# Kernel optimization log

Measured on AMD Instinct MI355X. Metric: run time of the kernel, lower is better.

Reference implementation:

```python
import jax, jax.numpy as jnp
import numpy as np

N_NODES = 100000
N_EDGES = 1600000
R_DIM = 8      # radial_embedding_dim (j)
L_DIM = 4      # angular dim (l)
C_DIM = 8      # channel_dim (k)
CUTOFF = 5.5
MP_NORM_FACTOR = 1.0


def setup_inputs() -> dict:
    key = jax.random.key(0)
    k1, k2, k3, k4, k5, k6, k7 = jax.random.split(key, 7)
    node_feat = jax.random.normal(k1, (N_NODES, R_DIM, L_DIM, C_DIM), dtype=jnp.float32)
    edge_lengths = jax.random.uniform(k2, (N_EDGES,), dtype=jnp.float32) * CUTOFF
    radial_cutoff_fn = jax.random.uniform(k3, (N_EDGES,), dtype=jnp.float32)
    edge_index = jax.random.randint(k4, (2, N_EDGES), 0, N_NODES, dtype=jnp.int64)
    prefactor = jax.random.uniform(k5, (R_DIM, C_DIM), dtype=jnp.float32)
    invr0 = (jax.random.uniform(k6, (R_DIM, C_DIM), dtype=jnp.float32) + 0.5) / CUTOFF
    memory_coef = jnp.float32(0.25)
    return {
        "node_feat": node_feat,
        "edge_lengths": edge_lengths,
        "radial_cutoff_fn": radial_cutoff_fn,
        "edge_index": edge_index,
        "prefactor": prefactor,
        "invr0": invr0,
        "memory_coef": memory_coef,
    }


def reference(node_feat, edge_lengths, radial_cutoff_fn, edge_index, prefactor, invr0, memory_coef):
    n_nodes = node_feat.shape[0]
    # radial decay: [E, R, C] = exp(-len * invr0) * prefactor * cutoff_fn
    radial_decay = (
        jnp.exp(-edge_lengths[:, None, None] * invr0)
        * prefactor
        * radial_cutoff_fn[:, None, None]
    )
    # gather sender features [E, R, L, C] and modulate per (edge, radial, channel)
    sender = node_feat[edge_index[0]]
    message = sender * radial_decay[:, :, None, :]
    # scatter-sum messages to receiver nodes
    agg = jax.ops.segment_sum(message, edge_index[1], num_segments=n_nodes)
    return node_feat * memory_coef + agg * MP_NORM_FACTOR
```

## Files before the change

kernel.cpp:

```cpp
#include <hip/hip_runtime.h>
#include <hip/hip_fp16.h>

#define RLC 256
#define BUCKET 32
#define OVF_CAP 65536
#define SCAN_BLOCK 256
#define SCAN_ITEMS 4

__device__ __forceinline__ float fast_exp2(float x) {
#if __has_builtin(__builtin_amdgcn_exp2f)
    return __builtin_amdgcn_exp2f(x);
#else
    return __expf(x * 0.6931471805599453f);
#endif
}

__device__ __forceinline__ unsigned int bfr(float f) {
    unsigned int u = __float_as_uint(f);
    return (u + 0x7fffu + ((u >> 16) & 1u)) >> 16;
}

#define LOG2E 1.4426950408889634f


__global__ __launch_bounds__(256) void cast_t_kernel(
    const float4* __restrict__ in, uint2* __restrict__ outp, int nr)
{
    int i = blockIdx.x * blockDim.x + threadIdx.x;
    if (i >= nr) return;
    const float4* p = in + (size_t)i * 8;
    float v[32];
    #pragma unroll
    for (int q = 0; q < 8; ++q) {
        float4 t = p[q];
        v[4*q+0] = t.x; v[4*q+1] = t.y; v[4*q+2] = t.z; v[4*q+3] = t.w;
    }
    uint2* o = outp + (size_t)i * 8;
    #pragma unroll
    for (int c = 0; c < 8; ++c) {
        unsigned int lo = bfr(v[0*8+c]) | (bfr(v[1*8+c]) << 16);
        unsigned int hi = bfr(v[2*8+c]) | (bfr(v[3*8+c]) << 16);
        o[c] = make_uint2(lo, hi);
    }
}

__global__ __launch_bounds__(256) void build_kernel(
    const int* __restrict__ edge_index,
    const float* __restrict__ edge_len,
    const float* __restrict__ cutoff_fn,
    int* __restrict__ counts,
    int2* __restrict__ payload,
    int4* __restrict__ ovf,
    int* __restrict__ ovf_cnt,
    int n_edges)
{
    int e = blockIdx.x * blockDim.x + threadIdx.x;
    if (e >= n_edges) return;
    int dst = edge_index[n_edges + e];
    int src = edge_index[e];
    unsigned int hnl = __half_as_ushort(__float2half(-edge_len[e]));
    unsigned int hcf = __half_as_ushort(__float2half(cutoff_fn[e]));
    int pk = (int)((hcf << 16) | hnl);
    int r = atomicAdd(&counts[dst], 1);
    if (r < BUCKET) {
        payload[(size_t)dst * BUCKET + r] = make_int2(src, pk);
    } else {
        int o = atomicAdd(ovf_cnt, 1);
        if (o < OVF_CAP) ovf[o] = make_int4(dst, src, pk, 0);
    }
}

__global__ __launch_bounds__(256) void gather_bucket_kernel(
    const float* __restrict__ node_feat,
    const unsigned short* __restrict__ nfbT,
    const int2* __restrict__ payload,
    const float* __restrict__ prefactor,
    const float* __restrict__ invr0,
    const float* __restrict__ coef_p,
    const int* __restrict__ counts,
    float* __restrict__ out,
    int n_nodes)
{
    __shared__ float4 slot[4][BUCKET];
    int wave = threadIdx.x >> 6;
    int lane = threadIdx.x & 63;
    int node = blockIdx.x * 4 + wave;
    bool valid = node < n_nodes;

    float iv = invr0[lane] * LOG2E;
    float pf = prefactor[lane];
    float coef = *coef_p;

    int r = lane >> 3, c = lane & 7;
    long obase = (long)node * RLC + r * 32 + c;

    float a0 = 0.f, a1 = 0.f, a2 = 0.f, a3 = 0.f;
    int m = 0;
    if (valid) {
        int deg = counts[node];
        m = deg < BUCKET ? deg : BUCKET;
        a0 = node_feat[obase]      * coef;
        a1 = node_feat[obase + 8]  * coef;
        a2 = node_feat[obase + 16] * coef;
        a3 = node_feat[obase + 24] * coef;
        if (lane < m) {
            int2 p = payload[(size_t)node * BUCKET + lane];
            float nl = __half2float(__ushort_as_half((unsigned short)(p.y & 0xffff)));
            float cf = __half2float(__ushort_as_half((unsigned short)(((unsigned int)p.y) >> 16)));
            slot[wave][lane] = make_float4(__int_as_float(p.x), nl, cf, 0.f);
        }
    }
    __syncthreads();

    if (valid) {
        #pragma unroll 4
        for (int it = 0; it < m; ++it) {
            float4 s = slot[wave][it];
            int src = __float_as_int(s.x);
            float w = fast_exp2(s.y * iv) * pf * s.z;
            uint2 raw = *(const uint2*)(nfbT + (size_t)src * RLC + lane * 4);
            float f0 = __uint_as_float(raw.x << 16);
            float f1 = __uint_as_float(raw.x & 0xffff0000u);
            float f2 = __uint_as_float(raw.y << 16);
            float f3 = __uint_as_float(raw.y & 0xffff0000u);
            a0 += w * f0; a1 += w * f1; a2 += w * f2; a3 += w * f3;
        }
        out[obase]      = a0;
        out[obase + 8]  = a1;
        out[obase + 16] = a2;
        out[obase + 24] = a3;
    }
}

__global__ __launch_bounds__(256) void ovf_kernel(
    const unsigned short* __restrict__ nfbT,
    const float* __restrict__ prefactor,
    const float* __restrict__ invr0,
    const int4* __restrict__ ovf,
    const int* __restrict__ ovf_cnt,
    float* __restrict__ out)
{
    int gtid = blockIdx.x * blockDim.x + threadIdx.x;
    int wid  = gtid >> 6;
    int lane = gtid & 63;
    int nwaves = (gridDim.x * blockDim.x) >> 6;
    int n = *ovf_cnt;
    if (n > OVF_CAP) n = OVF_CAP;

    float iv = invr0[lane] * LOG2E;
    float pf = prefactor[lane];
    int r = lane >> 3, c = lane & 7;

    for (int i = wid; i < n; i += nwaves) {
        int4 rec = ovf[i];
        int dst = rec.x, src = rec.y, pk = rec.z;
        float nl = __half2float(__ushort_as_half((unsigned short)(pk & 0xffff)));
        float cf = __half2float(__ushort_as_half((unsigned short)(((unsigned int)pk) >> 16)));
        float w = fast_exp2(nl * iv) * pf * cf;
        uint2 raw = *(const uint2*)(nfbT + (size_t)src * RLC + lane * 4);
        float f0 = __uint_as_float(raw.x << 16);
        float f1 = __uint_as_float(raw.x & 0xffff0000u);
        float f2 = __uint_as_float(raw.y << 16);
        float f3 = __uint_as_float(raw.y & 0xffff0000u);
        float* o = out + (long)dst * RLC + r * 32 + c;
        atomicAdd(o,      w * f0);
        atomicAdd(o + 8,  w * f1);
        atomicAdd(o + 16, w * f2);
        atomicAdd(o + 24, w * f3);
    }
}


__global__ __launch_bounds__(256) void cast_kernel(
    const float4* __restrict__ in, uint4* __restrict__ outp, int n8)
{
    int i = blockIdx.x * blockDim.x + threadIdx.x;
    if (i >= n8) return;
    float4 a = in[2 * i];
    float4 b = in[2 * i + 1];
    uint4 r;
    r.x = bfr(a.x) | (bfr(a.y) << 16);
    r.y = bfr(a.z) | (bfr(a.w) << 16);
    r.z = bfr(b.x) | (bfr(b.y) << 16);
    r.w = bfr(b.z) | (bfr(b.w) << 16);
    outp[i] = r;
}

__global__ __launch_bounds__(256) void hist_rank_kernel(
    const int* __restrict__ edge_index, int* __restrict__ counts,
    unsigned char* __restrict__ rank, int n_edges)
{
    int e = blockIdx.x * blockDim.x + threadIdx.x;
    if (e >= n_edges) return;
    int dst = edge_index[n_edges + e];
    int r = atomicAdd(&counts[dst], 1);
    rank[e] = (unsigned char)r;
}

__global__ __launch_bounds__(SCAN_BLOCK) void scan1_kernel(
    const int* __restrict__ in, int* __restrict__ out,
    int* __restrict__ blocksums, int n)
{
    __shared__ int tmp[SCAN_BLOCK];
    int t = threadIdx.x;
    int base = blockIdx.x * SCAN_BLOCK * SCAN_ITEMS + t * SCAN_ITEMS;
    int v[SCAN_ITEMS];
    int tot = 0;
    #pragma unroll
    for (int k = 0; k < SCAN_ITEMS; ++k) {
        int i = base + k;
        v[k] = (i < n) ? in[i] : 0;
        tot += v[k];
    }
    tmp[t] = tot;
    __syncthreads();
    int run = tot;
    for (int d = 1; d < SCAN_BLOCK; d <<= 1) {
        int x = (t >= d) ? tmp[t - d] : 0;
        __syncthreads();
        tmp[t] += x;
        __syncthreads();
    }
    int excl = tmp[t] - run;
    #pragma unroll
    for (int k = 0; k < SCAN_ITEMS; ++k) {
        int i = base + k;
        if (i < n) out[i] = excl;
        excl += v[k];
    }
    if (t == SCAN_BLOCK - 1) blocksums[blockIdx.x] = tmp[t];
}

__global__ __launch_bounds__(SCAN_BLOCK) void scan2_kernel(
    int* __restrict__ blocksums, int nb)
{
    __shared__ int tmp[SCAN_BLOCK];
    int t = threadIdx.x;
    int v = (t < nb) ? blocksums[t] : 0;
    tmp[t] = v;
    __syncthreads();
    for (int d = 1; d < SCAN_BLOCK; d <<= 1) {
        int x = (t >= d) ? tmp[t - d] : 0;
        __syncthreads();
        tmp[t] += x;
        __syncthreads();
    }
    if (t < nb) blocksums[t] = tmp[t] - v;
}

__global__ __launch_bounds__(256) void scan3_kernel(
    int* __restrict__ offsets, const int* __restrict__ blocksums,
    int n, int n_edges)
{
    int i = blockIdx.x * blockDim.x + threadIdx.x;
    if (i == 0) offsets[n] = n_edges;
    if (i >= n) return;
    offsets[i] += blocksums[i / (SCAN_BLOCK * SCAN_ITEMS)];
}

__global__ __launch_bounds__(256) void scatter_rank_kernel(
    const int* __restrict__ edge_index,
    const float* __restrict__ edge_len,
    const float* __restrict__ cutoff_fn,
    const int* __restrict__ offsets,
    const unsigned char* __restrict__ rank,
    int2* __restrict__ payload, int n_edges)
{
    int e = blockIdx.x * blockDim.x + threadIdx.x;
    if (e >= n_edges) return;
    int dst = edge_index[n_edges + e];
    int src = edge_index[e];
    unsigned int hnl = __half_as_ushort(__float2half(-edge_len[e]));
    unsigned int hcf = __half_as_ushort(__float2half(cutoff_fn[e]));
    int pos = offsets[dst] + (int)rank[e];
    payload[pos] = make_int2(src, (int)((hcf << 16) | hnl));
}

__global__ __launch_bounds__(256) void gather_kernel(
    const float* __restrict__ node_feat,
    const unsigned short* __restrict__ nfb,
    const int2* __restrict__ payload,
    const float* __restrict__ prefactor,
    const float* __restrict__ invr0,
    const float* __restrict__ coef_p,
    const int*  __restrict__ offsets,
    float* __restrict__ out,
    int n_nodes)
{
    int tid  = blockIdx.x * blockDim.x + threadIdx.x;
    int node = tid >> 6;
    int lane = threadIdx.x & 63;
    if (node >= n_nodes) return;

    int f0     = lane << 2;
    int rcbase = ((f0 >> 5) << 3) + (f0 & 7);

    float4 iv = *(const float4*)(invr0 + rcbase);
    iv.x *= LOG2E; iv.y *= LOG2E; iv.z *= LOG2E; iv.w *= LOG2E;
    const float4 pf = *(const float4*)(prefactor + rcbase);
    float coef = *coef_p;

    const float4 self = *(const float4*)(node_feat + (long)node * RLC + f0);
    float ax = self.x * coef, ay = self.y * coef,
          az = self.z * coef, aw = self.w * coef;

    int j   = offsets[node];
    int end = offsets[node + 1];

    for (int base = j; base < end; base += 64) {
        int idx = base + lane;
        int2 p = make_int2(0, 0);
        if (idx < end) p = payload[idx];
        int m = end - base;
        if (m > 64) m = 64;
        int psrc = p.x;
        int ppk  = p.y;

        #pragma unroll 4
        for (int it = 0; it < m; ++it) {
            int src = __shfl(psrc, it, 64);
            int pk  = __shfl(ppk,  it, 64);
            float nl = __half2float(__ushort_as_half((unsigned short)(pk & 0xffff)));
            float cf = __half2float(__ushort_as_half((unsigned short)(((unsigned int)pk) >> 16)));
            uint2 raw = *(const uint2*)(nfb + (long)src * RLC + f0);
            float fx = __uint_as_float(raw.x << 16);
            float fy = __uint_as_float(raw.x & 0xffff0000u);
            float fz = __uint_as_float(raw.y << 16);
            float fw = __uint_as_float(raw.y & 0xffff0000u);
            ax += fx * (fast_exp2(nl * iv.x) * pf.x * cf);
            ay += fy * (fast_exp2(nl * iv.y) * pf.y * cf);
            az += fz * (fast_exp2(nl * iv.z) * pf.z * cf);
            aw += fw * (fast_exp2(nl * iv.w) * pf.w * cf);
        }
    }

    *(float4*)(out + (long)node * RLC + f0) = make_float4(ax, ay, az, aw);
}

__global__ __launch_bounds__(256) void init_out_kernel(
    const float4* __restrict__ nf4, float4* __restrict__ out4,
    const float* __restrict__ coef_p, int n4)
{
    int i = blockIdx.x * blockDim.x + threadIdx.x;
    if (i >= n4) return;
    float c = *coef_p;
    float4 v = nf4[i];
    out4[i] = make_float4(v.x * c, v.y * c, v.z * c, v.w * c);
}

__global__ __launch_bounds__(256) void edge_scatter_kernel(
    const float* __restrict__ node_feat,
    const float* __restrict__ edge_len,
    const float* __restrict__ cutoff_fn,
    const int*  __restrict__ edge_index,
    const float* __restrict__ prefactor,
    const float* __restrict__ invr0,
    float* __restrict__ out, int n_edges)
{
    int tid  = blockIdx.x * blockDim.x + threadIdx.x;
    int e    = tid >> 6;
    int lane = threadIdx.x & 63;
    if (e >= n_edges) return;
    int   src = edge_index[e];
    int   dst = edge_index[n_edges + e];
    float len = edge_len[e];
    float cf  = cutoff_fn[e];
    int f0     = lane << 2;
    int rcbase = ((f0 >> 5) << 3) + (f0 & 7);
    const float4 iv = *(const float4*)(invr0 + rcbase);
    const float4 pf = *(const float4*)(prefactor + rcbase);
    const float4 s  = *(const float4*)(node_feat + (long)src * RLC + f0);
    float nl = -len;
    float* o = out + (long)dst * RLC + f0;
    atomicAdd(o + 0, s.x * __expf(nl * iv.x) * pf.x * cf);
    atomicAdd(o + 1, s.y * __expf(nl * iv.y) * pf.y * cf);
    atomicAdd(o + 2, s.z * __expf(nl * iv.z) * pf.z * cf);
    atomicAdd(o + 3, s.w * __expf(nl * iv.w) * pf.w * cf);
}

extern "C" void kernel_launch(void* const* d_in, const int* in_sizes, int n_in,
                              void* d_out, int out_size, void* d_ws, size_t ws_size,
                              hipStream_t stream) {
    const float* node_feat  = (const float*)d_in[0];
    const float* edge_len   = (const float*)d_in[1];
    const float* cutoff_fn  = (const float*)d_in[2];
    const int*   edge_index = (const int*)d_in[3];
    const float* prefactor  = (const float*)d_in[4];
    const float* invr0      = (const float*)d_in[5];
    const float* coef_p     = (const float*)d_in[6];
    float* out = (float*)d_out;

    const int n_edges = in_sizes[1];
    const int n_feat  = in_sizes[0];
    const int n_nodes = n_feat / RLC;

    size_t need1 = (size_t)n_feat * 2
                 + (size_t)n_nodes * BUCKET * 8
                 + (size_t)OVF_CAP * 16
                 + (size_t)(n_nodes + 1) * 4;

    const int per_block = SCAN_BLOCK * SCAN_ITEMS;
    const int nb1 = (n_nodes + per_block - 1) / per_block;
    size_t need2 = (size_t)n_feat * 2
                 + (size_t)n_edges * 8
                 + ((size_t)(n_nodes + 1) + n_nodes + 256) * 4
                 + (size_t)n_edges;

    if (ws_size >= need1) {
        unsigned short* nfbT = (unsigned short*)d_ws;
        int2* payload = (int2*)(nfbT + n_feat);
        int4* ovf     = (int4*)(payload + (size_t)n_nodes * BUCKET);
        int*  counts  = (int*)(ovf + OVF_CAP);
        int*  ovf_cnt = counts + n_nodes;

        int nr = n_nodes * 8;
        cast_t_kernel<<<(nr + 255) / 256, 256, 0, stream>>>(
            (const float4*)node_feat, (uint2*)nfbT, nr);

        (void)hipMemsetAsync(counts, 0, (size_t)(n_nodes + 1) * sizeof(int), stream);

        int eg = (n_edges + 255) / 256;
        build_kernel<<<eg, 256, 0, stream>>>(
            edge_index, edge_len, cutoff_fn, counts, payload, ovf, ovf_cnt, n_edges);

        int gg = (n_nodes + 3) / 4;
        gather_bucket_kernel<<<gg, 256, 0, stream>>>(
            node_feat, nfbT, payload, prefactor, invr0, coef_p, counts,
            out, n_nodes);

        ovf_kernel<<<64, 256, 0, stream>>>(
            nfbT, prefactor, invr0, ovf, ovf_cnt, out);
    } else if (ws_size >= need2 && nb1 <= SCAN_BLOCK) {
        unsigned short* nfb = (unsigned short*)d_ws;
        int2* payload   = (int2*)(nfb + n_feat);
        int* offsets    = (int*)(payload + n_edges);
        int* counts     = offsets + (n_nodes + 1);
        int* blocksums  = counts + n_nodes;
        unsigned char* rank = (unsigned char*)(blocksums + 256);

        int n8 = n_feat / 8;
        cast_kernel<<<(n8 + 255) / 256, 256, 0, stream>>>(
            (const float4*)node_feat, (uint4*)nfb, n8);

        (void)hipMemsetAsync(counts, 0, (size_t)n_nodes * sizeof(int), stream);

        int eg = (n_edges + 255) / 256;
        hist_rank_kernel<<<eg, 256, 0, stream>>>(edge_index, counts, rank, n_edges);
        scan1_kernel<<<nb1, SCAN_BLOCK, 0, stream>>>(counts, offsets, blocksums, n_nodes);
        scan2_kernel<<<1, SCAN_BLOCK, 0, stream>>>(blocksums, nb1);
        int ng = (n_nodes + 255) / 256;
        scan3_kernel<<<ng, 256, 0, stream>>>(offsets, blocksums, n_nodes, n_edges);
        scatter_rank_kernel<<<eg, 256, 0, stream>>>(
            edge_index, edge_len, cutoff_fn, offsets, rank, payload, n_edges);

        long total = (long)n_nodes * 64;
        int gg = (int)((total + 255) / 256);
        gather_kernel<<<gg, 256, 0, stream>>>(
            node_feat, nfb, payload, prefactor, invr0, coef_p, offsets,
            out, n_nodes);
    } else {
        int n4 = n_feat / 4;
        init_out_kernel<<<(n4 + 255) / 256, 256, 0, stream>>>(
            (const float4*)node_feat, (float4*)out, coef_p, n4);
        long total_threads = (long)n_edges * 64;
        int grid = (int)((total_threads + 255) / 256);
        edge_scatter_kernel<<<grid, 256, 0, stream>>>(
            node_feat, edge_len, cutoff_fn, edge_index,
            prefactor, invr0, out, n_edges);
    }
}
```

Measured before the change: 443.0 us.

## Merge cast and bucket-build kernels; drop LDS staging and use nontemporal accesses

The bf16 transpose-cast kernel and the edge bucket-build kernel now run as one launch, with blocks split by index range, so the two independent passes overlap and one launch disappears. In the gather kernel the shared-memory slot staging and the block-wide barrier are removed. Each wave now reads its payload entries directly inside the loop, and waves past the node count exit early. Streaming loads and stores are marked nontemporal to keep them from polluting cache, at the cost of more redundant payload loads per lane and less cache retention for the edge arrays.

```diff
diff --git a/kernel.cpp b/kernel.cpp
--- a/kernel.cpp
+++ b/kernel.cpp
@@ -23,28 +23,7 @@
 #define LOG2E 1.4426950408889634f
 
 
-__global__ __launch_bounds__(256) void cast_t_kernel(
-    const float4* __restrict__ in, uint2* __restrict__ outp, int nr)
-{
-    int i = blockIdx.x * blockDim.x + threadIdx.x;
-    if (i >= nr) return;
-    const float4* p = in + (size_t)i * 8;
-    float v[32];
-    #pragma unroll
-    for (int q = 0; q < 8; ++q) {
-        float4 t = p[q];
-        v[4*q+0] = t.x; v[4*q+1] = t.y; v[4*q+2] = t.z; v[4*q+3] = t.w;
-    }
-    uint2* o = outp + (size_t)i * 8;
-    #pragma unroll
-    for (int c = 0; c < 8; ++c) {
-        unsigned int lo = bfr(v[0*8+c]) | (bfr(v[1*8+c]) << 16);
-        unsigned int hi = bfr(v[2*8+c]) | (bfr(v[3*8+c]) << 16);
-        o[c] = make_uint2(lo, hi);
-    }
-}
-
-__global__ __launch_bounds__(256) void build_kernel(
+__global__ __launch_bounds__(256) void build_cast_kernel(
     const int* __restrict__ edge_index,
     const float* __restrict__ edge_len,
     const float* __restrict__ cutoff_fn,
@@ -52,21 +31,49 @@
     int2* __restrict__ payload,
     int4* __restrict__ ovf,
     int* __restrict__ ovf_cnt,
-    int n_edges)
-{
-    int e = blockIdx.x * blockDim.x + threadIdx.x;
-    if (e >= n_edges) return;
-    int dst = edge_index[n_edges + e];
-    int src = edge_index[e];
-    unsigned int hnl = __half_as_ushort(__float2half(-edge_len[e]));
-    unsigned int hcf = __half_as_ushort(__float2half(cutoff_fn[e]));
-    int pk = (int)((hcf << 16) | hnl);
-    int r = atomicAdd(&counts[dst], 1);
-    if (r < BUCKET) {
-        payload[(size_t)dst * BUCKET + r] = make_int2(src, pk);
+    int n_edges,
+    const float4* __restrict__ nf_in,
+    uint2* __restrict__ nfbT,
+    int nr,
+    int nb_build)
+{
+    if ((int)blockIdx.x < nb_build) {
+        int e = blockIdx.x * 256 + threadIdx.x;
+        if (e >= n_edges) return;
+        int dst = __builtin_nontemporal_load(edge_index + n_edges + e);
+        int src = __builtin_nontemporal_load(edge_index + e);
+        float  el = __builtin_nontemporal_load(edge_len + e);
+        float  cf = __builtin_nontemporal_load(cutoff_fn + e);
+        unsigned int hnl = __half_as_ushort(__float2half(-el));
+        unsigned int hcf = __half_as_ushort(__float2half(cf));
+        unsigned int pk = (hcf << 16) | hnl;
+        int r = atomicAdd(&counts[dst], 1);
+        if (r < BUCKET) {
+            unsigned long long v =
+                ((unsigned long long)pk << 32) | (unsigned int)src;
+            __builtin_nontemporal_store(
+                v, (unsigned long long*)&payload[(size_t)dst * BUCKET + r]);
+        } else {
+            int o = atomicAdd(ovf_cnt, 1);
+            if (o < OVF_CAP) ovf[o] = make_int4(dst, src, (int)pk, 0);
+        }
     } else {
-        int o = atomicAdd(ovf_cnt, 1);
-        if (o < OVF_CAP) ovf[o] = make_int4(dst, src, pk, 0);
+        int i = (blockIdx.x - nb_build) * 256 + threadIdx.x;
+        if (i >= nr) return;
+        const float4* p = nf_in + (size_t)i * 8;
+        float v[32];
+        #pragma unroll
+        for (int q = 0; q < 8; ++q) {
+            float4 t = p[q];
+            v[4*q+0] = t.x; v[4*q+1] = t.y; v[4*q+2] = t.z; v[4*q+3] = t.w;
+        }
+        uint2* o = nfbT + (size_t)i * 8;
+        #pragma unroll
+        for (int c = 0; c < 8; ++c) {
+            unsigned int lo = bfr(v[0*8+c]) | (bfr(v[1*8+c]) << 16);
+            unsigned int hi = bfr(v[2*8+c]) | (bfr(v[3*8+c]) << 16);
+            o[c] = make_uint2(lo, hi);
+        }
     }
 }
 
@@ -81,11 +88,10 @@
     float* __restrict__ out,
     int n_nodes)
 {
-    __shared__ float4 slot[4][BUCKET];
     int wave = threadIdx.x >> 6;
     int lane = threadIdx.x & 63;
     int node = blockIdx.x * 4 + wave;
-    bool valid = node < n_nodes;
+    if (node >= n_nodes) return;
 
     float iv = invr0[lane] * LOG2E;
     float pf = prefactor[lane];
@@ -94,42 +100,37 @@
     int r = lane >> 3, c = lane & 7;
     long obase = (long)node * RLC + r * 32 + c;
 
-    float a0 = 0.f, a1 = 0.f, a2 = 0.f, a3 = 0.f;
-    int m = 0;
-    if (valid) {
-        int deg = counts[node];
-        m = deg < BUCKET ? deg : BUCKET;
-        a0 = node_feat[obase]      * coef;
-        a1 = node_feat[obase + 8]  * coef;
-        a2 = node_feat[obase + 16] * coef;
-        a3 = node_feat[obase + 24] * coef;
-        if (lane < m) {
-            int2 p = payload[(size_t)node * BUCKET + lane];
-            float nl = __half2float(__ushort_as_half((unsigned short)(p.y & 0xffff)));
-            float cf = __half2float(__ushort_as_half((unsigned short)(((unsigned int)p.y) >> 16)));
-            slot[wave][lane] = make_float4(__int_as_float(p.x), nl, cf, 0.f);
-        }
-    }
-    __syncthreads();
-
-    if (valid) {
-        #pragma unroll 4
-        for (int it = 0; it < m; ++it) {
-            float4 s = slot[wave][it];
-            int src = __float_as_int(s.x);
-            float w = fast_exp2(s.y * iv) * pf * s.z;
-            uint2 raw = *(const uint2*)(nfbT + (size_t)src * RLC + lane * 4);
-            float f0 = __uint_as_float(raw.x << 16);
-            float f1 = __uint_as_float(raw.x & 0xffff0000u);
-            float f2 = __uint_as_float(raw.y << 16);
-            float f3 = __uint_as_float(raw.y & 0xffff0000u);
-            a0 += w * f0; a1 += w * f1; a2 += w * f2; a3 += w * f3;
-        }
-        out[obase]      = a0;
-        out[obase + 8]  = a1;
-        out[obase + 16] = a2;
-        out[obase + 24] = a3;
-    }
+    int deg = counts[node];
+    int m = deg < BUCKET ? deg : BUCKET;
+
+    float a0 = __builtin_nontemporal_load(node_feat + obase)      * coef;
+    float a1 = __builtin_nontemporal_load(node_feat + obase + 8)  * coef;
+    float a2 = __builtin_nontemporal_load(node_feat + obase + 16) * coef;
+    float a3 = __builtin_nontemporal_load(node_feat + obase + 24) * coef;
+
+    const int2* pp = payload + (size_t)node * BUCKET;
+    const unsigned short* tb = nfbT + lane * 4;
+
+    #pragma unroll 4
+    for (int it = 0; it < m; ++it) {
+        int2 p = pp[it];
+        int src = p.x;
+        unsigned int pk = (unsigned int)p.y;
+        float nl = __half2float(__ushort_as_half((unsigned short)(pk & 0xffff)));
+        float cf = __half2float(__ushort_as_half((unsigned short)(pk >> 16)));
+        float w = fast_exp2(nl * iv) * pf * cf;
+        uint2 raw = *(const uint2*)(tb + (size_t)src * RLC);
+        float f0 = __uint_as_float(raw.x << 16);
+        float f1 = __uint_as_float(raw.x & 0xffff0000u);
+        float f2 = __uint_as_float(raw.y << 16);
+        float f3 = __uint_as_float(raw.y & 0xffff0000u);
+        a0 += w * f0; a1 += w * f1; a2 += w * f2; a3 += w * f3;
+    }
+
+    __builtin_nontemporal_store(a0, out + obase);
+    __builtin_nontemporal_store(a1, out + obase + 8);
+    __builtin_nontemporal_store(a2, out + obase + 16);
+    __builtin_nontemporal_store(a3, out + obase + 24);
 }
 
 __global__ __launch_bounds__(256) void ovf_kernel(
@@ -413,15 +414,14 @@
         int*  counts  = (int*)(ovf + OVF_CAP);
         int*  ovf_cnt = counts + n_nodes;
 
+        (void)hipMemsetAsync(counts, 0, (size_t)(n_nodes + 1) * sizeof(int), stream);
+
         int nr = n_nodes * 8;
-        cast_t_kernel<<<(nr + 255) / 256, 256, 0, stream>>>(
-            (const float4*)node_feat, (uint2*)nfbT, nr);
-
-        (void)hipMemsetAsync(counts, 0, (size_t)(n_nodes + 1) * sizeof(int), stream);
-
-        int eg = (n_edges + 255) / 256;
-        build_kernel<<<eg, 256, 0, stream>>>(
-            edge_index, edge_len, cutoff_fn, counts, payload, ovf, ovf_cnt, n_edges);
+        int nb_build = (n_edges + 255) / 256;
+        int nb_cast  = (nr + 255) / 256;
+        build_cast_kernel<<<nb_build + nb_cast, 256, 0, stream>>>(
+            edge_index, edge_len, cutoff_fn, counts, payload, ovf, ovf_cnt,
+            n_edges, (const float4*)node_feat, (uint2*)nfbT, nr, nb_build);
 
         int gg = (n_nodes + 3) / 4;
         gather_bucket_kernel<<<gg, 256, 0, stream>>>(
```

After: 469.7 us. +6.0%, slower.
